# Kernel optimization log

Measured on AMD Instinct MI355X. Metric: run time of the kernel, lower is better.

The kernel has to match this reference:

```python
import jax, jax.numpy as jnp
import numpy as np

B, N, S, C, H = 16, 64, 4096, 768, 1
HEAD_DIM = C // H
SCALE = HEAD_DIM ** -0.5
ASSIGN_EPS = 1.0


def setup_inputs() -> dict:
    key = jax.random.key(0)
    ks = jax.random.split(key, 8)
    w = lambda k: jax.random.normal(k, (C, C), jnp.float32) * 0.02
    return {
        "query": jax.random.normal(ks[0], (B, N, C), jnp.float32),       # group tokens
        "key_tokens": jax.random.normal(ks[1], (B, S, C), jnp.float32),  # sequence tokens
        "Wq": w(ks[2]), "bq": jnp.zeros((C,), jnp.float32),
        "Wk": w(ks[3]), "bk": jnp.zeros((C,), jnp.float32),
        "Wv": w(ks[4]), "bv": jnp.zeros((C,), jnp.float32),
        "Wo": w(ks[5]), "bo": jnp.zeros((C,), jnp.float32),
    }


def reference(query, key_tokens, Wq, bq, Wk, bk, Wv, bv, Wo, bo):
    # AssignAttention forward (hard=True, gumbel=False -> hard_softmax path).
    def split_heads(x):  # [b, t, C] -> [b, h, t, c]
        b, t, _ = x.shape
        return x.reshape(b, t, H, HEAD_DIM).transpose(0, 2, 1, 3)

    q = split_heads(query @ Wq.T + bq)        # [B, H, N, c]
    k = split_heads(key_tokens @ Wk.T + bk)   # [B, H, S, c]
    v = split_heads(key_tokens @ Wv.T + bv)   # [B, H, S, c]

    raw_attn = jnp.einsum('bhnc,bhsc->bhns', q, k) * SCALE  # [B, H, N, S]

    # hard_softmax over the group (query) dim, axis=-2, with straight-through estimator
    y_soft = jax.nn.softmax(raw_attn, axis=-2)
    idx = jnp.argmax(y_soft, axis=-2)                          # [B, H, S]
    y_hard = jnp.swapaxes(jax.nn.one_hot(idx, N, dtype=raw_attn.dtype), -1, -2)  # [B, H, N, S]
    attn = jax.lax.stop_gradient(y_hard - y_soft) + y_soft

    # sum-renormalization over assigned tokens (sum_assign=False)
    attn = attn / (attn.sum(axis=-1, keepdims=True) + ASSIGN_EPS)

    out = jnp.einsum('bhns,bhsc->bhnc', attn, v)  # [B, H, N, c]
    out = out.transpose(0, 2, 1, 3).reshape(B, N, C)
    return out @ Wo.T + bo
```

## Files before the change

kernel.cpp:

```cpp
#include <hip/hip_runtime.h>
#include <hip/hip_bf16.h>

#define BQ 16
#define NG 64
#define SQ 4096
#define CD 768
#define ROWS (BQ*NG)
#define KSP 4

__global__ __launch_bounds__(256)
void transpose64(const float* __restrict__ src, float* __restrict__ dst,
                 int M, int N)
{
    __shared__ float t[64][65];
    const int bx = blockIdx.x * 64;
    const int by = blockIdx.y * 64;
    const int tx = threadIdx.x & 63, tw = threadIdx.x >> 6;
#pragma unroll
    for (int i = 0; i < 16; ++i) {
        const int row = i * 4 + tw;
        t[row][tx] = src[(size_t)(by + row) * N + bx + tx];
    }
    __syncthreads();
#pragma unroll
    for (int i = 0; i < 16; ++i) {
        const int row = i * 4 + tw;
        dst[(size_t)(bx + row) * M + by + tx] = t[tx][row];
    }
}

__global__ __launch_bounds__(256)
void vecmat3(const float* __restrict__ Wq, const float* __restrict__ bk,
             const float* __restrict__ Wk, const float* __restrict__ bq,
             const float* __restrict__ WoT, const float* __restrict__ bv,
             float* __restrict__ uq, float* __restrict__ bqk,
             float* __restrict__ bvo)
{
    __shared__ float red[4][64];
    const float* Mm; const float* v; float* out;
    if (blockIdx.y == 0)      { Mm = Wq;  v = bk; out = uq;  }
    else if (blockIdx.y == 1) { Mm = Wk;  v = bq; out = bqk; }
    else                      { Mm = WoT; v = bv; out = bvo; }
    const int j0 = blockIdx.x * 64;
    const int jl = threadIdx.x & 63;
    const int cs = threadIdx.x >> 6;
    double a = 0.0;
    for (int c = cs; c < CD; c += 4)
        a += (double)Mm[(size_t)c * CD + j0 + jl] * (double)v[c];
    red[cs][jl] = (float)a;
    __syncthreads();
    if (cs == 0) out[j0 + jl] = red[0][jl] + red[1][jl] + red[2][jl] + red[3][jl];
}

__global__ __launch_bounds__(256)
void delta_q(const float* __restrict__ query, const float* __restrict__ uq,
             const float* __restrict__ bq, const float* __restrict__ bk,
             double* __restrict__ delta)
{
    const int r    = blockIdx.x * 4 + (threadIdx.x >> 6);
    const int lane = threadIdx.x & 63;
    double a = 0.0, b = 0.0;
    for (int c = lane; c < CD; c += 64) {
        a += (double)query[(size_t)r * CD + c] * (double)uq[c];
        b += (double)bq[c] * (double)bk[c];
    }
    a += b;
    for (int off = 32; off; off >>= 1) a += __shfl_down(a, off, 64);
    if (lane == 0) delta[r] = a;
}

__device__ __forceinline__
void gemm_core(const float* __restrict__ AT, int lda,
               const float* __restrict__ B,  int ldb,
               float* __restrict__ Pz, int r0, int c0, int k0, int prow0)
{
    __shared__ float As[64][72];
    __shared__ float Bs[64][72];
    const int tid = threadIdx.x;
    const int c4  = tid & 15;
    const int kr  = tid >> 4;
    const int cg  = tid & 15;
    const int rg  = tid >> 4;

    float  acc[4][4]; double acc64[4][4];
#pragma unroll
    for (int i = 0; i < 4; ++i)
#pragma unroll
        for (int j = 0; j < 4; ++j) { acc[i][j] = 0.f; acc64[i][j] = 0.0; }

    for (int ch = 0; ch < 3; ++ch) {
        const int kb = k0 + ch * 64;
        if (ch) __syncthreads();
#pragma unroll
        for (int i = 0; i < 4; ++i) {
            const int row = i * 16 + kr;
            *(float4*)&As[row][4 * c4] = *(const float4*)(AT + (size_t)(kb + row) * lda + r0 + 4 * c4);
            *(float4*)&Bs[row][4 * c4] = *(const float4*)(B  + (size_t)(kb + row) * ldb + c0 + 4 * c4);
        }
        __syncthreads();
#pragma unroll 8
        for (int dd = 0; dd < 64; ++dd) {
            const float4 a = *(const float4*)&As[dd][4 * rg];
            const float4 b = *(const float4*)&Bs[dd][4 * cg];
            const float av[4] = {a.x, a.y, a.z, a.w};
            const float bv[4] = {b.x, b.y, b.z, b.w};
#pragma unroll
            for (int i = 0; i < 4; ++i)
#pragma unroll
                for (int j = 0; j < 4; ++j) acc[i][j] += av[i] * bv[j];
        }
#pragma unroll
        for (int i = 0; i < 4; ++i)
#pragma unroll
            for (int j = 0; j < 4; ++j) { acc64[i][j] += (double)acc[i][j]; acc[i][j] = 0.f; }
    }
#pragma unroll
    for (int i = 0; i < 4; ++i) {
        const int row = prow0 + 4 * rg + i;
        float4 v;
        v.x = (float)acc64[i][0]; v.y = (float)acc64[i][1];
        v.z = (float)acc64[i][2]; v.w = (float)acc64[i][3];
        *(float4*)(Pz + (size_t)row * CD + c0 + 4 * cg) = v;
    }
}

__global__ __launch_bounds__(256)
void gemm_w(const float* __restrict__ Wq, const float* __restrict__ Wk,
            const float* __restrict__ Wv, const float* __restrict__ WoT,
            float* __restrict__ P)
{
    const int by = blockIdx.y;
    float* Pz = P + (size_t)blockIdx.z * (1536 * CD);
    const float* AT; const float* Bp; int r0;
    if (by < 12) { AT = Wq; Bp = Wk;  r0 = by * 64; }
    else         { AT = Wv; Bp = WoT; r0 = (by - 12) * 64; }
    gemm_core(AT, CD, Bp, CD, Pz, r0, blockIdx.x * 64, blockIdx.z * 192, by * 64);
}

__global__ __launch_bounds__(256)
void gemm_d(const float* __restrict__ AT, const float* __restrict__ B,
            float* __restrict__ P)
{
    float* Pz = P + (size_t)blockIdx.z * (ROWS * CD);
    const int r0 = blockIdx.y * 64;
    gemm_core(AT, ROWS, B, CD, Pz, r0, blockIdx.x * 64, blockIdx.z * 192, r0);
}

__global__ __launch_bounds__(256)
void reduce_sk(const float* __restrict__ P, const float* __restrict__ bias,
               const float* __restrict__ bias2, const int* __restrict__ cnt,
               float* __restrict__ out, int M, int mode)
{
    const int e = blockIdx.x * 256 + threadIdx.x;
    if (e >= M * CD) return;
    const size_t MN = (size_t)M * CD;
    double a = 0.0;
#pragma unroll
    for (int z = 0; z < KSP; ++z) a += (double)P[z * MN + e];
    float v = (float)a;
    if (mode == 1) v += bias[e % CD];
    else if (mode == 3) {
        const int r = e / CD;
        const int cv = cnt[r];
        const float invf = 1.f / ((float)cv + 1.f);
        v = v * invf + ((float)cv * invf) * bias2[e % CD] + bias[e % CD];
    }
    out[e] = v;
}

struct ScoreTiles { float gt[64][68]; float ktA[64][64]; float ktB[64][64]; };
struct ScoreRed   { double bval[128][17]; int bidx[128][17]; };
union  ScoreShared { ScoreTiles t; ScoreRed r; };

__global__ __launch_bounds__(256)
void score_argmax(const float* __restrict__ g, const float* __restrict__ key,
                  const double* __restrict__ delta, int* __restrict__ idxo)
{
    __shared__ alignas(16) ScoreShared sh;
    __shared__ double dl[64];
    const int tid  = threadIdx.x;
    const int b    = blockIdx.y;
    const int s0   = blockIdx.x * 128;
    const int sg   = tid & 15;
    const int ng   = tid >> 4;
    const int lrow = tid >> 4;
    const int c4   = tid & 15;

    if (tid < 64) dl[tid] = delta[b * 64 + tid];

    float  accC[4][8];
    double acc64[4][8];
#pragma unroll
    for (int i = 0; i < 4; ++i)
#pragma unroll
        for (int j = 0; j < 8; ++j) { accC[i][j] = 0.f; acc64[i][j] = 0.0; }

    for (int kc = 0; kc < CD; kc += 64) {
#pragma unroll
        for (int p = 0; p < 4; ++p) {
            const int nrow = p * 16 + lrow;
            const float4 v = *(const float4*)(g + (size_t)(b * 64 + nrow) * CD + kc + 4 * c4);
            sh.t.gt[4*c4+0][nrow] = v.x; sh.t.gt[4*c4+1][nrow] = v.y;
            sh.t.gt[4*c4+2][nrow] = v.z; sh.t.gt[4*c4+3][nrow] = v.w;
        }
#pragma unroll
        for (int p = 0; p < 8; ++p) {
            const int srow = p * 16 + lrow;
            const float4 v = *(const float4*)(key + (size_t)(b * SQ + s0 + srow) * CD + kc + 4 * c4);
            const int gs = srow >> 3;
            const int lo = srow & 3;
            const bool hi = (srow & 4) != 0;
            const float vv[4] = { v.x, v.y, v.z, v.w };
#pragma unroll
            for (int i = 0; i < 4; ++i) {
                const int dd = 4 * c4 + i;
                const int col = (((gs + dd) & 15) << 2) + lo;
                if (hi) sh.t.ktB[dd][col] = vv[i];
                else    sh.t.ktA[dd][col] = vv[i];
            }
        }
        __syncthreads();
#pragma unroll 4
        for (int dd = 0; dd < 64; ++dd) {
            const int cA = ((sg + dd) & 15) << 2;
            const float4 ga = *(const float4*)&sh.t.gt[dd][4 * ng];
            const float4 k0 = *(const float4*)&sh.t.ktA[dd][cA];
            const float4 k1 = *(const float4*)&sh.t.ktB[dd][cA];
            const float gs_[4] = { ga.x, ga.y, ga.z, ga.w };
            const float ks[8] = { k0.x, k0.y, k0.z, k0.w, k1.x, k1.y, k1.z, k1.w };
#pragma unroll
            for (int i = 0; i < 4; ++i)
#pragma unroll
                for (int j = 0; j < 8; ++j) accC[i][j] += gs_[i] * ks[j];
        }
        __syncthreads();
#pragma unroll
        for (int i = 0; i < 4; ++i)
#pragma unroll
            for (int j = 0; j < 8; ++j) { acc64[i][j] += (double)accC[i][j]; accC[i][j] = 0.f; }
    }

    double bv[8]; int bn[8];
#pragma unroll
    for (int j = 0; j < 8; ++j) {
        bv[j] = acc64[0][j] + dl[4 * ng + 0]; bn[j] = 4 * ng + 0;
#pragma unroll
        for (int i = 1; i < 4; ++i) {
            const double v = acc64[i][j] + dl[4 * ng + i];
            if (v > bv[j]) { bv[j] = v; bn[j] = 4 * ng + i; }
        }
    }
    __syncthreads();
#pragma unroll
    for (int j = 0; j < 8; ++j) {
        sh.r.bval[8 * sg + j][ng] = bv[j];
        sh.r.bidx[8 * sg + j][ng] = bn[j];
    }
    __syncthreads();
    if (tid < 128) {
        const int s = tid;
        double best = sh.r.bval[s][0]; int bi = sh.r.bidx[s][0];
        for (int k = 1; k < 16; ++k) {
            const double v = sh.r.bval[s][k];
            if (v > best) { best = v; bi = sh.r.bidx[s][k]; }
        }
        idxo[b * SQ + s0 + s] = bi;
    }
}

__global__ __launch_bounds__(256)
void gather_ksum(const float* __restrict__ key, const int* __restrict__ idx,
                 float* __restrict__ Ksum, int* __restrict__ cnt)
{
    __shared__ int slist[SQ];
    __shared__ int scount;
    const int n   = blockIdx.x;
    const int b   = blockIdx.y;
    const int tid = threadIdx.x;
    if (tid == 0) scount = 0;
    __syncthreads();

    const int* ib = idx + b * SQ;
#pragma unroll
    for (int p = 0; p < SQ / 256; ++p) {
        const int s = p * 256 + tid;
        if (ib[s] == n) {
            const int pos = atomicAdd(&scount, 1);
            slist[pos] = s;
        }
    }
    __syncthreads();
    const int m = scount;

    double a0 = 0.0, a1 = 0.0, a2 = 0.0;
    const float* kb = key + (size_t)b * SQ * CD;
    const int c1 = tid + 256, c2 = tid + 512;

    int r = 0;
    for (; r + 4 <= m; r += 4) {
        const float* p0 = kb + (size_t)slist[r]     * CD;
        const float* p1 = kb + (size_t)slist[r + 1] * CD;
        const float* p2 = kb + (size_t)slist[r + 2] * CD;
        const float* p3 = kb + (size_t)slist[r + 3] * CD;
        a0 += (double)p0[tid] + (double)p1[tid] + (double)p2[tid] + (double)p3[tid];
        a1 += (double)p0[c1] + (double)p1[c1] + (double)p2[c1] + (double)p3[c1];
        a2 += (double)p0[c2] + (double)p1[c2] + (double)p2[c2] + (double)p3[c2];
    }
    for (; r < m; ++r) {
        const float* p0 = kb + (size_t)slist[r] * CD;
        a0 += (double)p0[tid]; a1 += (double)p0[c1]; a2 += (double)p0[c2];
    }

    float* out = Ksum + (size_t)(b * 64 + n) * CD;
    out[tid] = (float)a0; out[c1] = (float)a1; out[c2] = (float)a2;
    if (tid == 0) cnt[b * 64 + n] = m;
}

extern "C" void kernel_launch(void* const* d_in, const int* in_sizes, int n_in,
                              void* d_out, int out_size, void* d_ws, size_t ws_size,
                              hipStream_t stream)
{
    const float* query = (const float*)d_in[0];
    const float* key   = (const float*)d_in[1];
    const float* Wq    = (const float*)d_in[2];
    const float* bq    = (const float*)d_in[3];
    const float* Wk    = (const float*)d_in[4];
    const float* bk    = (const float*)d_in[5];
    const float* Wv    = (const float*)d_in[6];
    const float* bv    = (const float*)d_in[7];
    const float* Wo    = (const float*)d_in[8];
    const float* bo    = (const float*)d_in[9];

    char* ws = (char*)d_ws;
    const size_t MB = 1 << 20;
    int*    cnt   = (int*)   (ws + 0);
    double* delta = (double*)(ws + 4096);
    float*  uq    = (float*) (ws + 16384);
    float*  bqk   = (float*) (ws + 19456);
    float*  bvo   = (float*) (ws + 22528);
    int*    idx   = (int*)   (ws + 32768);
    float*  qT    = (float*) (ws + 1 * MB);
    float*  WoT   = (float*) (ws + 4 * MB);
    float*  Wqk   = (float*) (ws + 7 * MB);
    float*  Wvo   = Wqk + 768 * 768;
    float*  g     = (float*) (ws + 12 * MB);
    float*  Ksum  = (float*) (ws + 15 * MB);
    float*  KsumT = (float*) (ws + 18 * MB);
    float*  P     = (float*) (ws + 21 * MB);

    transpose64<<<dim3(12, 12), 256, 0, stream>>>(Wo, WoT, CD, CD);
    transpose64<<<dim3(12, 16), 256, 0, stream>>>(query, qT, ROWS, CD);
    vecmat3<<<dim3(12, 3), 256, 0, stream>>>(Wq, bk, Wk, bq, WoT, bv, uq, bqk, bvo);
    delta_q<<<ROWS / 4, 256, 0, stream>>>(query, uq, bq, bk, delta);
    gemm_w<<<dim3(12, 24, KSP), 256, 0, stream>>>(Wq, Wk, Wv, WoT, P);
    reduce_sk<<<(1536 * CD) / 256, 256, 0, stream>>>(P, nullptr, nullptr, nullptr, Wqk, 1536, 0);
    gemm_d<<<dim3(12, 16, KSP), 256, 0, stream>>>(qT, Wqk, P);
    reduce_sk<<<(ROWS * CD) / 256, 256, 0, stream>>>(P, bqk, nullptr, nullptr, g, ROWS, 1);
    score_argmax<<<dim3(SQ / 128, BQ), 256, 0, stream>>>(g, key, delta, idx);
    gather_ksum<<<dim3(NG, BQ), 256, 0, stream>>>(key, idx, Ksum, cnt);
    transpose64<<<dim3(12, 16), 256, 0, stream>>>(Ksum, KsumT, ROWS, CD);
    gemm_d<<<dim3(12, 16, KSP), 256, 0, stream>>>(KsumT, Wvo, P);
    reduce_sk<<<(ROWS * CD) / 256, 256, 0, stream>>>(P, bo, bvo, cnt, (float*)d_out, ROWS, 3);
}
```

Measured before the change: 578.6 us.

## Retile score_argmax to 8x8 per-thread tiles with register-prefetched double buffering

The score/argmax kernel is rewritten to use 128 threads, each computing an 8x8 tile of group-by-sequence scores instead of 4x8. The next K-chunk is prefetched into registers while the current one is computed, and the key tile uses an XOR-swizzled shared layout. An extra transpose of g is added so the A operand can be loaded with coalesced float4 reads. The aim is more reuse per shared-memory load and hidden global latency, at the cost of heavier register pressure, one extra kernel launch, and fewer threads per block.

```diff
diff --git a/kernel.cpp b/kernel.cpp
--- a/kernel.cpp
+++ b/kernel.cpp
@@ -168,86 +168,99 @@
     out[e] = v;
 }
 
-struct ScoreTiles { float gt[64][68]; float ktA[64][64]; float ktB[64][64]; };
-struct ScoreRed   { double bval[128][17]; int bidx[128][17]; };
+struct ScoreTiles { float As[64][64]; float Bs[128][64]; };
+struct ScoreRed   { double bval[128][9]; int bidx[128][9]; };
 union  ScoreShared { ScoreTiles t; ScoreRed r; };
 
-__global__ __launch_bounds__(256)
-void score_argmax(const float* __restrict__ g, const float* __restrict__ key,
+__global__ __launch_bounds__(128, 1)
+void score_argmax(const float* __restrict__ gT, const float* __restrict__ key,
                   const double* __restrict__ delta, int* __restrict__ idxo)
 {
-    __shared__ alignas(16) ScoreShared sh;
+    __shared__ ScoreShared sh;
     __shared__ double dl[64];
-    const int tid  = threadIdx.x;
-    const int b    = blockIdx.y;
-    const int s0   = blockIdx.x * 128;
-    const int sg   = tid & 15;
-    const int ng   = tid >> 4;
-    const int lrow = tid >> 4;
-    const int c4   = tid & 15;
+    const int tid = threadIdx.x;
+    const int b   = blockIdx.y;
+    const int s0  = blockIdx.x * 128;
+    const int sg  = tid & 15;
+    const int ng  = tid >> 4;
+    const int c4  = tid & 15;
+    const int t4  = tid >> 4;
 
     if (tid < 64) dl[tid] = delta[b * 64 + tid];
 
-    float  accC[4][8];
-    double acc64[4][8];
-#pragma unroll
-    for (int i = 0; i < 4; ++i)
-#pragma unroll
-        for (int j = 0; j < 8; ++j) { accC[i][j] = 0.f; acc64[i][j] = 0.0; }
-
-    for (int kc = 0; kc < CD; kc += 64) {
-#pragma unroll
-        for (int p = 0; p < 4; ++p) {
-            const int nrow = p * 16 + lrow;
-            const float4 v = *(const float4*)(g + (size_t)(b * 64 + nrow) * CD + kc + 4 * c4);
-            sh.t.gt[4*c4+0][nrow] = v.x; sh.t.gt[4*c4+1][nrow] = v.y;
-            sh.t.gt[4*c4+2][nrow] = v.z; sh.t.gt[4*c4+3][nrow] = v.w;
-        }
-#pragma unroll
-        for (int p = 0; p < 8; ++p) {
-            const int srow = p * 16 + lrow;
-            const float4 v = *(const float4*)(key + (size_t)(b * SQ + s0 + srow) * CD + kc + 4 * c4);
-            const int gs = srow >> 3;
-            const int lo = srow & 3;
-            const bool hi = (srow & 4) != 0;
-            const float vv[4] = { v.x, v.y, v.z, v.w };
-#pragma unroll
-            for (int i = 0; i < 4; ++i) {
-                const int dd = 4 * c4 + i;
-                const int col = (((gs + dd) & 15) << 2) + lo;
-                if (hi) sh.t.ktB[dd][col] = vv[i];
-                else    sh.t.ktA[dd][col] = vv[i];
+    float  acc[8][8]; double acc64[8][8];
+#pragma unroll
+    for (int i = 0; i < 8; ++i)
+#pragma unroll
+        for (int j = 0; j < 8; ++j) { acc[i][j] = 0.f; acc64[i][j] = 0.0; }
+
+    float4 ra[8];
+    float4 rb[16];
+    const float* gTb  = gT  + (size_t)b * 64 + 4 * c4;
+    const float* keyb = key + ((size_t)b * SQ + s0) * CD + 4 * c4;
+
+#pragma unroll
+    for (int q = 0; q < 8; ++q)
+        ra[q] = *(const float4*)(gTb + (size_t)(8 * q + t4) * ROWS);
+#pragma unroll
+    for (int p = 0; p < 16; ++p)
+        rb[p] = *(const float4*)(keyb + (size_t)(8 * p + t4) * CD);
+
+    for (int t = 0; t < 12; ++t) {
+        __syncthreads();
+#pragma unroll
+        for (int q = 0; q < 8; ++q)
+            *(float4*)&sh.t.As[8 * q + t4][4 * c4] = ra[q];
+#pragma unroll
+        for (int p = 0; p < 16; ++p)
+            *(float4*)&sh.t.Bs[8 * p + t4][4 * (c4 ^ p)] = rb[p];
+        __syncthreads();
+        if (t < 11) {
+            const int kc = (t + 1) * 64;
+            const float* ga = gTb + (size_t)kc * ROWS;
+            const float* ka = keyb + kc;
+#pragma unroll
+            for (int q = 0; q < 8; ++q)
+                ra[q] = *(const float4*)(ga + (size_t)(8 * q + t4) * ROWS);
+#pragma unroll
+            for (int p = 0; p < 16; ++p)
+                rb[p] = *(const float4*)(ka + (size_t)(8 * p + t4) * CD);
+        }
+#pragma unroll 4
+        for (int ddq = 0; ddq < 16; ++ddq) {
+            float4 kf[8];
+            const int xc = ((ddq ^ sg) & 15) << 2;
+#pragma unroll
+            for (int j = 0; j < 8; ++j)
+                kf[j] = *(const float4*)&sh.t.Bs[8 * sg + j][xc];
+#pragma unroll
+            for (int d = 0; d < 4; ++d) {
+                const float4 a0 = *(const float4*)&sh.t.As[4 * ddq + d][8 * ng];
+                const float4 a1 = *(const float4*)&sh.t.As[4 * ddq + d][8 * ng + 4];
+                const float av[8] = { a0.x, a0.y, a0.z, a0.w, a1.x, a1.y, a1.z, a1.w };
+#pragma unroll
+                for (int j = 0; j < 8; ++j) {
+                    const float kd = (d == 0) ? kf[j].x : (d == 1) ? kf[j].y
+                                   : (d == 2) ? kf[j].z : kf[j].w;
+#pragma unroll
+                    for (int i = 0; i < 8; ++i) acc[i][j] += av[i] * kd;
+                }
             }
         }
-        __syncthreads();
-#pragma unroll 4
-        for (int dd = 0; dd < 64; ++dd) {
-            const int cA = ((sg + dd) & 15) << 2;
-            const float4 ga = *(const float4*)&sh.t.gt[dd][4 * ng];
-            const float4 k0 = *(const float4*)&sh.t.ktA[dd][cA];
-            const float4 k1 = *(const float4*)&sh.t.ktB[dd][cA];
-            const float gs_[4] = { ga.x, ga.y, ga.z, ga.w };
-            const float ks[8] = { k0.x, k0.y, k0.z, k0.w, k1.x, k1.y, k1.z, k1.w };
-#pragma unroll
-            for (int i = 0; i < 4; ++i)
-#pragma unroll
-                for (int j = 0; j < 8; ++j) accC[i][j] += gs_[i] * ks[j];
-        }
-        __syncthreads();
-#pragma unroll
-        for (int i = 0; i < 4; ++i)
-#pragma unroll
-            for (int j = 0; j < 8; ++j) { acc64[i][j] += (double)accC[i][j]; accC[i][j] = 0.f; }
+#pragma unroll
+        for (int i = 0; i < 8; ++i)
+#pragma unroll
+            for (int j = 0; j < 8; ++j) { acc64[i][j] += (double)acc[i][j]; acc[i][j] = 0.f; }
     }
 
     double bv[8]; int bn[8];
 #pragma unroll
     for (int j = 0; j < 8; ++j) {
-        bv[j] = acc64[0][j] + dl[4 * ng + 0]; bn[j] = 4 * ng + 0;
-#pragma unroll
-        for (int i = 1; i < 4; ++i) {
-            const double v = acc64[i][j] + dl[4 * ng + i];
-            if (v > bv[j]) { bv[j] = v; bn[j] = 4 * ng + i; }
+        bv[j] = acc64[0][j] + dl[8 * ng + 0]; bn[j] = 8 * ng;
+#pragma unroll
+        for (int i = 1; i < 8; ++i) {
+            const double v = acc64[i][j] + dl[8 * ng + i];
+            if (v > bv[j]) { bv[j] = v; bn[j] = 8 * ng + i; }
         }
     }
     __syncthreads();
@@ -257,10 +270,11 @@
         sh.r.bidx[8 * sg + j][ng] = bn[j];
     }
     __syncthreads();
-    if (tid < 128) {
+    {
         const int s = tid;
         double best = sh.r.bval[s][0]; int bi = sh.r.bidx[s][0];
-        for (int k = 1; k < 16; ++k) {
+#pragma unroll
+        for (int k = 1; k < 8; ++k) {
             const double v = sh.r.bval[s][k];
             if (v > best) { best = v; bi = sh.r.bidx[s][k]; }
         }
@@ -356,7 +370,9 @@
     reduce_sk<<<(1536 * CD) / 256, 256, 0, stream>>>(P, nullptr, nullptr, nullptr, Wqk, 1536, 0);
     gemm_d<<<dim3(12, 16, KSP), 256, 0, stream>>>(qT, Wqk, P);
     reduce_sk<<<(ROWS * CD) / 256, 256, 0, stream>>>(P, bqk, nullptr, nullptr, g, ROWS, 1);
-    score_argmax<<<dim3(SQ / 128, BQ), 256, 0, stream>>>(g, key, delta, idx);
+    float* gT = qT;
+    transpose64<<<dim3(12, 16), 256, 0, stream>>>(g, gT, ROWS, CD);
+    score_argmax<<<dim3(SQ / 128, BQ), 128, 0, stream>>>(gT, key, delta, idx);
     gather_ksum<<<dim3(NG, BQ), 256, 0, stream>>>(key, idx, Ksum, cnt);
     transpose64<<<dim3(12, 16), 256, 0, stream>>>(Ksum, KsumT, ROWS, CD);
     gemm_d<<<dim3(12, 16, KSP), 256, 0, stream>>>(KsumT, Wvo, P);
```

New measurement: 715.1 us. +23.6%, slower.
